# Performance work log

Hardware: AMD Instinct MI355X
Metric: run time of the kernel (lower is better)

The kernel has to match this reference:

```python
import jax, jax.numpy as jnp
import numpy as np

N = 12288  # points in image 0
M = 12288  # points in image 1
D = 128    # descriptor dim
TEMP_SQRT_INV = 1.0 / np.sqrt(0.1)  # temperature = 0.1, applied to each descriptor


def setup_inputs() -> dict:
    key = jax.random.key(0)
    k0, k1, k2, k3, k4, k5 = jax.random.split(key, 6)
    desc_0 = jax.random.normal(k0, (N, D), jnp.float32)
    desc_0 = desc_0 / jnp.linalg.norm(desc_0, axis=-1, keepdims=True)
    desc_1 = jax.random.normal(k1, (M, D), jnp.float32)
    desc_1 = desc_1 / jnp.linalg.norm(desc_1, axis=-1, keepdims=True)
    # correspondence indices; -1 means "no correspondence"
    corr_0 = jax.random.randint(k2, (N,), -1, M, dtype=jnp.int64 if jax.config.jax_enable_x64 else jnp.int32)
    corr_1 = jax.random.randint(k3, (M,), -1, N, dtype=jnp.int64 if jax.config.jax_enable_x64 else jnp.int32)
    logits_0 = jax.random.normal(k4, (N,), jnp.float32)
    logits_1 = jax.random.normal(k5, (M,), jnp.float32)
    return {"desc_0": desc_0, "desc_1": desc_1, "corr_0": corr_0,
            "corr_1": corr_1, "logits_0": logits_0, "logits_1": logits_1}


def reference(desc_0, desc_1, corr_0, corr_1, logits_0, logits_1):
    # temperature scaling (module scales both descriptor sets by 1/sqrt(T))
    d0 = desc_0 * TEMP_SQRT_INV
    d1 = desc_1 * TEMP_SQRT_INV
    # dense similarity matrix [N, M] (the blockwise kernel target)
    S = jnp.einsum('nd,md->nm', d0, d1)

    m0 = corr_0 >= 0
    m1 = corr_1 >= 0
    i0 = jnp.clip(corr_0, 0)
    i1 = jnp.clip(corr_1, 0)

    # bidirectional InfoNCE cross-entropy (rows for image0, cols for image1)
    lse_0 = jax.nn.logsumexp(S, axis=1)               # [N]
    lse_1 = jax.nn.logsumexp(S, axis=0)               # [M]
    pos_0 = jnp.take_along_axis(S, i0[:, None], axis=1)[:, 0]  # S[i, corr_0[i]]
    pos_1 = S[i1, jnp.arange(M)]                                # S[corr_1[j], j]
    l0 = jnp.where(m0, lse_0 - pos_0, 0.0)
    l1 = jnp.where(m1, lse_1 - pos_1, 0.0)
    loss_0 = l0.sum() / jnp.maximum(m0.sum(), 1)
    loss_1 = l1.sum() / jnp.maximum(m1.sum(), 1)

    # mutual-nearest-neighbor matching + logit-gated precision/recall
    best_0 = jnp.argmax(S, axis=1)                    # [N] best match in image 1
    best_1 = jnp.argmax(S, axis=0)                    # [M] best match in image 0
    mutual = best_1[best_0] == jnp.arange(N)
    kp0 = jax.nn.sigmoid(logits_0) >= 0.5
    kp1 = jax.nn.sigmoid(logits_1) >= 0.5
    predicted = mutual & kp0 & kp1[best_0]
    correct = (best_0 == corr_0) & m0
    tp = (correct & predicted).sum()
    precision = tp / jnp.maximum(predicted.sum(), 1)
    recall = tp / jnp.maximum(m0.sum(), 1)
    return loss_0, loss_1, precision, recall
```

## Files before the change

### kernel.cpp

```cpp
#include <hip/hip_runtime.h>
#include <hip/hip_bf16.h>

#define NPTS 12288
#define DD 128
#define CHUNKS 16
#define CHW (NPTS / CHUNKS)
#define TILES (CHW / 64)
#define NBG (NPTS / 128)

#define PRESCALE 3.79828262f

typedef short bf16x8 __attribute__((ext_vector_type(8)));
typedef float f32x4 __attribute__((ext_vector_type(4)));

__device__ __forceinline__ float fast_exp2(float x) {
#if defined(__has_builtin)
#if __has_builtin(__builtin_amdgcn_exp2f)
  return __builtin_amdgcn_exp2f(x);
#else
  return exp2f(x);
#endif
#else
  return exp2f(x);
#endif
}

__device__ __forceinline__ short f2bf(float f) {
  unsigned u = __float_as_uint(f);
  u += 0x7FFFu + ((u >> 16) & 1u);
  return (short)(u >> 16);
}

__device__ __forceinline__ unsigned umax(unsigned a, unsigned b) { return a > b ? a : b; }

__global__ void k_conv(const float* __restrict__ d0, const float* __restrict__ d1,
                       short* __restrict__ o0, short* __restrict__ o1) {
  unsigned t = blockIdx.x * 256u + threadIdx.x;
  const unsigned half = (NPTS * DD) / 4;
  const float* src; short* dst; unsigned g;
  if (t < half) { src = d0; dst = o0; g = t; }
  else          { src = d1; dst = o1; g = t - half; }
  float4 v = *(const float4*)(src + (size_t)g * 4);
  short4 r;
  r.x = f2bf(v.x * PRESCALE); r.y = f2bf(v.y * PRESCALE);
  r.z = f2bf(v.z * PRESCALE); r.w = f2bf(v.w * PRESCALE);
  *(short4*)(dst + (size_t)g * 4) = r;
}

__launch_bounds__(256, 3)
__global__ void k_main(const short* __restrict__ d0b, const short* __restrict__ d1b,
                       uint2* __restrict__ colKV, uint2* __restrict__ rowKV) {
  __shared__ __align__(16) char bLds[2][16384];
  __shared__ uint2 crLds[2][4][64];
  const int widx = threadIdx.x >> 6;
  const int lane = threadIdx.x & 63;
  const int lo = lane & 15, hi = lane >> 4;
  const int chunk = blockIdx.x & (CHUNKS - 1);
  const int bg = blockIdx.x >> 4;
  const int row0 = bg * 128 + widx * 32;
  const int cbase = chunk * CHW;

  const char* btile0 = (const char*)(d1b + (size_t)cbase * DD);

  #define STAGE(tt, bb) do {                                                   \
    const char* gsrc_ = btile0 + (size_t)(tt) * 16384;                         \
    _Pragma("unroll")                                                          \
    for (int it_ = 0; it_ < 4; it_++) {                                        \
      int L_ = (widx << 12) + (it_ << 10) + (lane << 4);                       \
      int so_ = L_ ^ (((L_ >> 8) & 7) << 4);                                   \
      __builtin_amdgcn_global_load_lds((const void*)(gsrc_ + so_),             \
          (void*)(&bLds[bb][(widx << 12) + (it_ << 10)]), 16, 0, 0);           \
    }                                                                          \
  } while (0)

  bf16x8 af[2][4];
  #pragma unroll
  for (int i = 0; i < 2; i++)
    #pragma unroll
    for (int kk = 0; kk < 4; kk++)
      af[i][kk] = *(const bf16x8*)(d0b + (size_t)(row0 + i * 16 + lo) * DD + kk * 32 + hi * 8);

  float rowsum[2][4], rowkeyf[2][4];
  #pragma unroll
  for (int i = 0; i < 2; i++)
    #pragma unroll
    for (int r = 0; r < 4; r++) {
      rowsum[i][r] = 0.f;
      rowkeyf[i][r] = 0.f;
    }
  const unsigned rcbase = 0x3FFFu - (unsigned)(row0 + hi * 4);
  const int axor = (lo & 7) << 4;

  STAGE(0, 0);
  __syncthreads();

  #pragma unroll 1
  for (int t = 0; t < TILES; t++) {
    const int cur = t & 1;
    if (t + 1 < TILES) STAGE(t + 1, cur ^ 1);

    f32x4 acc[2][4];
    #pragma unroll
    for (int i = 0; i < 2; i++)
      #pragma unroll
      for (int j = 0; j < 4; j++)
        acc[i][j] = (f32x4){0.f, 0.f, 0.f, 0.f};

    const char* bbuf = &bLds[cur][0];
    #pragma unroll
    for (int kk = 0; kk < 4; kk++) {
      bf16x8 bfr[4];
      #pragma unroll
      for (int j = 0; j < 4; j++) {
        int bbyte = (((j << 4) + lo) << 8) + (kk << 6) + (hi << 4);
        bbyte ^= axor;
        bfr[j] = *(const bf16x8*)(bbuf + bbyte);
      }
      #pragma unroll
      for (int j = 0; j < 4; j++)
        #pragma unroll
        for (int i = 0; i < 2; i++)
          acc[i][j] = __builtin_amdgcn_mfma_f32_16x16x32_bf16(af[i][kk], bfr[j], acc[i][j], 0, 0, 0);
    }

    const int ct = cbase + t * 64;
    #pragma unroll
    for (int j = 0; j < 4; j++) {
      float colsum = 0.f;
      float colkeyf = 0.f;
      const unsigned ccomp = 0x3FFFu - (unsigned)(ct + j * 16 + lo);
      #pragma unroll
      for (int i = 0; i < 2; i++)
        #pragma unroll
        for (int r = 0; r < 4; r++) {
          float e = fast_exp2(acc[i][j][r]);
          unsigned tb = __float_as_uint(e) & 0xFFFFC000u;
          rowkeyf[i][r] = fmaxf(rowkeyf[i][r], __uint_as_float(tb | ccomp));
          colkeyf = fmaxf(colkeyf, __uint_as_float(tb | (rcbase - (unsigned)(i * 16 + r))));
          rowsum[i][r] += e;
          colsum += e;
        }
      colsum += __shfl_xor(colsum, 16, 64);
      colsum += __shfl_xor(colsum, 32, 64);
      colkeyf = fmaxf(colkeyf, __shfl_xor(colkeyf, 16, 64));
      colkeyf = fmaxf(colkeyf, __shfl_xor(colkeyf, 32, 64));
      if (hi == 0)
        crLds[cur][widx][j * 16 + lo] = make_uint2(__float_as_uint(colkeyf), __float_as_uint(colsum));
    }

    __syncthreads();

    if (lo < 16 && hi == 0) { }
    if (lane < 16) {
      int c = widx * 16 + lane;
      uint2 p0 = crLds[cur][0][c], p1 = crLds[cur][1][c];
      uint2 p2 = crLds[cur][2][c], p3 = crLds[cur][3][c];
      float s = __uint_as_float(p0.y) + __uint_as_float(p1.y) +
                __uint_as_float(p2.y) + __uint_as_float(p3.y);
      float k = fmaxf(fmaxf(__uint_as_float(p0.x), __uint_as_float(p1.x)),
                      fmaxf(__uint_as_float(p2.x), __uint_as_float(p3.x)));
      colKV[(size_t)bg * NPTS + ct + c] = make_uint2(__float_as_uint(k), __float_as_uint(s));
    }
  }

  #pragma unroll
  for (int i = 0; i < 2; i++)
    #pragma unroll
    for (int r = 0; r < 4; r++) {
      float s = rowsum[i][r];
      float k = rowkeyf[i][r];
      s += __shfl_xor(s, 1, 64); s += __shfl_xor(s, 2, 64);
      s += __shfl_xor(s, 4, 64); s += __shfl_xor(s, 8, 64);
      k = fmaxf(k, __shfl_xor(k, 1, 64));
      k = fmaxf(k, __shfl_xor(k, 2, 64));
      k = fmaxf(k, __shfl_xor(k, 4, 64));
      k = fmaxf(k, __shfl_xor(k, 8, 64));
      if (lo == 0) {
        int row = row0 + i * 16 + hi * 4 + r;
        rowKV[(size_t)chunk * NPTS + row] = make_uint2(__float_as_uint(k), __float_as_uint(s));
      }
    }
  #undef STAGE
}

__global__ void k_red(const uint2* __restrict__ colKV, const uint2* __restrict__ rowKV,
                      const float* __restrict__ d0, const float* __restrict__ d1,
                      const int* __restrict__ c0, const int* __restrict__ c1,
                      unsigned* __restrict__ best0, unsigned* __restrict__ best1,
                      float* __restrict__ l0part, float* __restrict__ l1part) {
  float v;
  if (blockIdx.x < 48) {
    int m = blockIdx.x * 256 + threadIdx.x;
    float s = 0.f; unsigned k = 0u;
    #pragma unroll 8
    for (int b = 0; b < NBG; b++) {
      uint2 kv = colKV[(size_t)b * NPTS + m];
      s += __uint_as_float(kv.y);
      k = umax(k, kv.x);
    }
    best1[m] = 0x3FFFu - (k & 0x3FFFu);
    int cc = c1[m];
    int i = cc > 0 ? cc : 0;
    const float4* pa = (const float4*)(d0 + (size_t)i * DD);
    const float4* pb = (const float4*)(d1 + (size_t)m * DD);
    float dot = 0.f;
    #pragma unroll 8
    for (int q = 0; q < DD / 4; q++) {
      float4 a = pa[q], b = pb[q];
      dot += a.x * b.x + a.y * b.y + a.z * b.z + a.w * b.w;
    }
    v = (cc >= 0) ? (logf(s) - 10.0f * dot) : 0.f;
  } else {
    int n = (blockIdx.x - 48) * 256 + threadIdx.x;
    float s = 0.f; unsigned k = 0u;
    #pragma unroll
    for (int c = 0; c < CHUNKS; c++) {
      uint2 kv = rowKV[(size_t)c * NPTS + n];
      s += __uint_as_float(kv.y);
      k = umax(k, kv.x);
    }
    best0[n] = 0x3FFFu - (k & 0x3FFFu);
    int cc = c0[n];
    int i = cc > 0 ? cc : 0;
    const float4* pa = (const float4*)(d0 + (size_t)n * DD);
    const float4* pb = (const float4*)(d1 + (size_t)i * DD);
    float dot = 0.f;
    #pragma unroll 8
    for (int q = 0; q < DD / 4; q++) {
      float4 a = pa[q], b = pb[q];
      dot += a.x * b.x + a.y * b.y + a.z * b.z + a.w * b.w;
    }
    v = (cc >= 0) ? (logf(s) - 10.0f * dot) : 0.f;
  }
  __shared__ float red[256];
  red[threadIdx.x] = v; __syncthreads();
  for (int st = 128; st > 0; st >>= 1) {
    if (threadIdx.x < st) red[threadIdx.x] += red[threadIdx.x + st];
    __syncthreads();
  }
  if (threadIdx.x == 0) {
    if (blockIdx.x < 48) l1part[blockIdx.x] = red[0];
    else                 l0part[blockIdx.x - 48] = red[0];
  }
}

__global__ void k_stats(const int* __restrict__ c0, const int* __restrict__ c1,
                        const float* __restrict__ lg0, const float* __restrict__ lg1,
                        const unsigned* __restrict__ best0, const unsigned* __restrict__ best1,
                        int4* __restrict__ statpart) {
  int n = blockIdx.x * 256 + threadIdx.x;
  int cc = c0[n];
  bool m0 = cc >= 0;
  int b0 = (int)best0[n];
  bool mutual = ((int)best1[b0] == n);
  bool pred = mutual && (lg0[n] >= 0.f) && (lg1[b0] >= 0.f);
  int4 v;
  v.x = m0 ? 1 : 0;
  v.y = (c1[n] >= 0) ? 1 : 0;
  v.z = (pred && m0 && b0 == cc) ? 1 : 0;
  v.w = pred ? 1 : 0;
  __shared__ int4 red[256];
  red[threadIdx.x] = v; __syncthreads();
  for (int st = 128; st > 0; st >>= 1) {
    if (threadIdx.x < st) {
      int4 o = red[threadIdx.x + st];
      red[threadIdx.x].x += o.x; red[threadIdx.x].y += o.y;
      red[threadIdx.x].z += o.z; red[threadIdx.x].w += o.w;
    }
    __syncthreads();
  }
  if (threadIdx.x == 0) statpart[blockIdx.x] = red[0];
}

__global__ void k_final(const float* __restrict__ l0part, const float* __restrict__ l1part,
                        const int4* __restrict__ statpart, float* __restrict__ out) {
  const int tid = threadIdx.x;
  float l0s = 0.f, l1s = 0.f;
  int4 st = make_int4(0, 0, 0, 0);
  if (tid < 48) {
    l0s = l0part[tid]; l1s = l1part[tid];
    st = statpart[tid];
  }
  #pragma unroll
  for (int off = 32; off >= 1; off >>= 1) {
    l0s += __shfl_down(l0s, off, 64);
    l1s += __shfl_down(l1s, off, 64);
    st.x += __shfl_down(st.x, off, 64);
    st.y += __shfl_down(st.y, off, 64);
    st.z += __shfl_down(st.z, off, 64);
    st.w += __shfl_down(st.w, off, 64);
  }
  if (tid == 0) {
    int M0 = st.x > 0 ? st.x : 1;
    int M1 = st.y > 0 ? st.y : 1;
    int PR = st.w > 0 ? st.w : 1;
    out[0] = l0s / (float)M0;
    out[1] = l1s / (float)M1;
    out[2] = (float)st.z / (float)PR;
    out[3] = (float)st.z / (float)M0;
  }
}

extern "C" void kernel_launch(void* const* d_in, const int* in_sizes, int n_in,
                              void* d_out, int out_size, void* d_ws, size_t ws_size,
                              hipStream_t stream) {
  const float* desc0 = (const float*)d_in[0];
  const float* desc1 = (const float*)d_in[1];
  const int* corr0   = (const int*)d_in[2];
  const int* corr1   = (const int*)d_in[3];
  const float* lg0   = (const float*)d_in[4];
  const float* lg1   = (const float*)d_in[5];
  float* out = (float*)d_out;

  char* w = (char*)d_ws;
  short* d0b   = (short*)(w);
  short* d1b   = (short*)(w + 3145728);
  uint2* colKV = (uint2*)(w + 6291456);
  uint2* rowKV = (uint2*)(w + 15728640);
  unsigned* best0 = (unsigned*)(w + 17301504);
  unsigned* best1 = (unsigned*)(w + 17350656);
  float* l0part = (float*)(w + 17399808);
  float* l1part = (float*)(w + 17400000);
  int4* statpart = (int4*)(w + 17400192);

  k_conv<<<3072, 256, 0, stream>>>(desc0, desc1, d0b, d1b);
  k_main<<<1536, 256, 0, stream>>>(d0b, d1b, colKV, rowKV);
  k_red<<<96, 256, 0, stream>>>(colKV, rowKV, desc0, desc1, corr0, corr1, best0, best1, l0part, l1part);
  k_stats<<<48, 256, 0, stream>>>(corr0, corr1, lg0, lg1, best0, best1, statpart);
  k_final<<<1, 64, 0, stream>>>(l0part, l1part, statpart, out);
}
```

Measured before the change: 104.0 us.

## Software-pipeline MFMA tile with previous tile's exp epilogue using dual accumulators

Restructures the tile loop into a two-stage software pipeline: the MFMA for tile t+1 is issued into a second accumulator set while the exp/max/sum epilogue of tile t runs, and the cross-wave column combine is delayed by one tile. The aim is to hide MFMA latency behind the transcendental and shuffle work and to cut barrier stalls. The cost is doubled accumulator registers, which may lower occupancy, plus a hard-coded unrolled schedule that assumes TILES == 12.

```diff
diff --git a/kernel.cpp b/kernel.cpp
--- a/kernel.cpp
+++ b/kernel.cpp
@@ -91,77 +91,104 @@
   const unsigned rcbase = 0x3FFFu - (unsigned)(row0 + hi * 4);
   const int axor = (lo & 7) << 4;
 
+  f32x4 accA[2][4], accB[2][4];
+
+  #define MFMA_STEP(ACC, CUR) do {                                             \
+    _Pragma("unroll")                                                          \
+    for (int i_ = 0; i_ < 2; i_++)                                             \
+      _Pragma("unroll")                                                        \
+      for (int j_ = 0; j_ < 4; j_++)                                           \
+        ACC[i_][j_] = (f32x4){0.f, 0.f, 0.f, 0.f};                             \
+    const char* bbuf_ = &bLds[CUR][0];                                         \
+    _Pragma("unroll")                                                          \
+    for (int kk_ = 0; kk_ < 4; kk_++) {                                        \
+      bf16x8 bfr_[4];                                                          \
+      _Pragma("unroll")                                                        \
+      for (int j_ = 0; j_ < 4; j_++) {                                         \
+        int bb_ = (((j_ << 4) + lo) << 8) + (kk_ << 6) + (hi << 4);            \
+        bb_ ^= axor;                                                           \
+        bfr_[j_] = *(const bf16x8*)(bbuf_ + bb_);                              \
+      }                                                                        \
+      _Pragma("unroll")                                                        \
+      for (int j_ = 0; j_ < 4; j_++)                                           \
+        _Pragma("unroll")                                                      \
+        for (int i_ = 0; i_ < 2; i_++)                                         \
+          ACC[i_][j_] = __builtin_amdgcn_mfma_f32_16x16x32_bf16(               \
+              af[i_][kk_], bfr_[j_], ACC[i_][j_], 0, 0, 0);                    \
+    }                                                                          \
+  } while (0)
+
+  #define EPI_STEP(ACC, TT) do {                                               \
+    const int ct_ = cbase + (TT) * 64;                                         \
+    _Pragma("unroll")                                                          \
+    for (int j_ = 0; j_ < 4; j_++) {                                           \
+      float colsum_ = 0.f, colkey_ = 0.f;                                      \
+      const unsigned ccomp_ = 0x3FFFu - (unsigned)(ct_ + j_ * 16 + lo);        \
+      _Pragma("unroll")                                                        \
+      for (int i_ = 0; i_ < 2; i_++)                                           \
+        _Pragma("unroll")                                                      \
+        for (int r_ = 0; r_ < 4; r_++) {                                       \
+          float e_ = fast_exp2(ACC[i_][j_][r_]);                               \
+          unsigned tb_ = __float_as_uint(e_) & 0xFFFFC000u;                    \
+          rowkeyf[i_][r_] = fmaxf(rowkeyf[i_][r_], __uint_as_float(tb_ | ccomp_)); \
+          colkey_ = fmaxf(colkey_, __uint_as_float(tb_ | (rcbase - (unsigned)(i_ * 16 + r_)))); \
+          rowsum[i_][r_] += e_;                                                \
+          colsum_ += e_;                                                       \
+        }                                                                      \
+      colsum_ += __shfl_xor(colsum_, 16, 64);                                  \
+      colsum_ += __shfl_xor(colsum_, 32, 64);                                  \
+      colkey_ = fmaxf(colkey_, __shfl_xor(colkey_, 16, 64));                   \
+      colkey_ = fmaxf(colkey_, __shfl_xor(colkey_, 32, 64));                   \
+      if (hi == 0)                                                             \
+        crLds[(TT) & 1][widx][j_ * 16 + lo] =                                  \
+            make_uint2(__float_as_uint(colkey_), __float_as_uint(colsum_));    \
+    }                                                                          \
+  } while (0)
+
+  #define COMBINE(TT) do {                                                     \
+    if ((TT) >= 0 && lane < 16) {                                              \
+      int c_ = widx * 16 + lane;                                               \
+      const int p_ = (TT) & 1;                                                 \
+      uint2 p0_ = crLds[p_][0][c_], p1_ = crLds[p_][1][c_];                    \
+      uint2 p2_ = crLds[p_][2][c_], p3_ = crLds[p_][3][c_];                    \
+      float s_ = __uint_as_float(p0_.y) + __uint_as_float(p1_.y) +             \
+                 __uint_as_float(p2_.y) + __uint_as_float(p3_.y);              \
+      float k_ = fmaxf(fmaxf(__uint_as_float(p0_.x), __uint_as_float(p1_.x)),  \
+                       fmaxf(__uint_as_float(p2_.x), __uint_as_float(p3_.x))); \
+      colKV[(size_t)bg * NPTS + cbase + (TT) * 64 + c_] =                      \
+          make_uint2(__float_as_uint(k_), __float_as_uint(s_));                \
+    }                                                                          \
+  } while (0)
+
   STAGE(0, 0);
   __syncthreads();
+  STAGE(1, 1);
+  MFMA_STEP(accA, 0);
 
   #pragma unroll 1
-  for (int t = 0; t < TILES; t++) {
-    const int cur = t & 1;
-    if (t + 1 < TILES) STAGE(t + 1, cur ^ 1);
-
-    f32x4 acc[2][4];
-    #pragma unroll
-    for (int i = 0; i < 2; i++)
-      #pragma unroll
-      for (int j = 0; j < 4; j++)
-        acc[i][j] = (f32x4){0.f, 0.f, 0.f, 0.f};
-
-    const char* bbuf = &bLds[cur][0];
-    #pragma unroll
-    for (int kk = 0; kk < 4; kk++) {
-      bf16x8 bfr[4];
-      #pragma unroll
-      for (int j = 0; j < 4; j++) {
-        int bbyte = (((j << 4) + lo) << 8) + (kk << 6) + (hi << 4);
-        bbyte ^= axor;
-        bfr[j] = *(const bf16x8*)(bbuf + bbyte);
-      }
-      #pragma unroll
-      for (int j = 0; j < 4; j++)
-        #pragma unroll
-        for (int i = 0; i < 2; i++)
-          acc[i][j] = __builtin_amdgcn_mfma_f32_16x16x32_bf16(af[i][kk], bfr[j], acc[i][j], 0, 0, 0);
-    }
-
-    const int ct = cbase + t * 64;
-    #pragma unroll
-    for (int j = 0; j < 4; j++) {
-      float colsum = 0.f;
-      float colkeyf = 0.f;
-      const unsigned ccomp = 0x3FFFu - (unsigned)(ct + j * 16 + lo);
-      #pragma unroll
-      for (int i = 0; i < 2; i++)
-        #pragma unroll
-        for (int r = 0; r < 4; r++) {
-          float e = fast_exp2(acc[i][j][r]);
-          unsigned tb = __float_as_uint(e) & 0xFFFFC000u;
-          rowkeyf[i][r] = fmaxf(rowkeyf[i][r], __uint_as_float(tb | ccomp));
-          colkeyf = fmaxf(colkeyf, __uint_as_float(tb | (rcbase - (unsigned)(i * 16 + r))));
-          rowsum[i][r] += e;
-          colsum += e;
-        }
-      colsum += __shfl_xor(colsum, 16, 64);
-      colsum += __shfl_xor(colsum, 32, 64);
-      colkeyf = fmaxf(colkeyf, __shfl_xor(colkeyf, 16, 64));
-      colkeyf = fmaxf(colkeyf, __shfl_xor(colkeyf, 32, 64));
-      if (hi == 0)
-        crLds[cur][widx][j * 16 + lo] = make_uint2(__float_as_uint(colkeyf), __float_as_uint(colsum));
-    }
-
+  for (int k = 0; k < 5; k++) {
+    const int o = 2 * k + 1;
     __syncthreads();
-
-    if (lo < 16 && hi == 0) { }
-    if (lane < 16) {
-      int c = widx * 16 + lane;
-      uint2 p0 = crLds[cur][0][c], p1 = crLds[cur][1][c];
-      uint2 p2 = crLds[cur][2][c], p3 = crLds[cur][3][c];
-      float s = __uint_as_float(p0.y) + __uint_as_float(p1.y) +
-                __uint_as_float(p2.y) + __uint_as_float(p3.y);
-      float k = fmaxf(fmaxf(__uint_as_float(p0.x), __uint_as_float(p1.x)),
-                      fmaxf(__uint_as_float(p2.x), __uint_as_float(p3.x)));
-      colKV[(size_t)bg * NPTS + ct + c] = make_uint2(__float_as_uint(k), __float_as_uint(s));
-    }
-  }
+    STAGE(o + 1, 0);
+    MFMA_STEP(accB, 1);
+    EPI_STEP(accA, o - 1);
+    COMBINE(2 * k - 1);
+    __syncthreads();
+    if (o + 2 < TILES) STAGE(o + 2, 1);
+    MFMA_STEP(accA, 0);
+    EPI_STEP(accB, o);
+    COMBINE(2 * k);
+  }
+
+  __syncthreads();
+  MFMA_STEP(accB, 1);
+  EPI_STEP(accA, 10);
+  COMBINE(9);
+  __syncthreads();
+  EPI_STEP(accB, 11);
+  __syncthreads();
+  COMBINE(10);
+  COMBINE(11);
 
   #pragma unroll
   for (int i = 0; i < 2; i++)
@@ -181,6 +208,9 @@
       }
     }
   #undef STAGE
+  #undef MFMA_STEP
+  #undef EPI_STEP
+  #undef COMBINE
 }
 
 __global__ void k_red(const uint2* __restrict__ colKV, const uint2* __restrict__ rowKV,
```

Result: slower. 283.9 us (+173.0%).
